# Kernel tuning notes

Hardware: AMD Instinct MI355X
Metric: run time of the kernel (lower is better)

## Reference

```python
import jax, jax.numpy as jnp
import numpy as np

NUM_BITS = 16           # continuousVarEncodingNumBits
THRESH = 4.0            # segmentActivationThreshold
K_SYN = 32              # numberOfSynapsesPerSegment
B, F, H, C = 512, 128, 8192, 10
E = F * NUM_BITS        # encodedFeatureSize = 2048


def _make_weight(key, n, p):
    # Dense int8-style weights: ~K_SYN random +/-1 synapses per neuron, rest 0.
    k1, k2 = jax.random.split(key)
    signs = jnp.where(jax.random.bernoulli(k1, 0.5, (n, p)), 1.0, -1.0)
    mask = jax.random.bernoulli(k2, K_SYN / p, (n, p))
    return (signs * mask).astype(jnp.float32)


def setup_inputs() -> dict:
    key = jax.random.key(0)
    ks = jax.random.split(key, 6)
    x = jax.random.uniform(ks[0], (B, F), dtype=jnp.float32)
    W0 = _make_weight(ks[1], H, E)   # layer 0: hidden x encoded
    W1 = _make_weight(ks[2], H, H)
    W2 = _make_weight(ks[3], H, H)
    # output connection matrix (numberOfHiddenLayers, hidden, classes); float variant
    outConn = jax.random.uniform(ks[4], (3, H, C), dtype=jnp.float32)
    return {"trainOrTest": 0, "x": x, "W0": W0, "W1": W1, "W2": W2, "outConn": outConn}


def reference(trainOrTest, x, W0, W1, W2, outConn):
    # thermometer bit-encoding of continuous vars: bit j on if x*NUM_BITS > j
    levels = jnp.arange(NUM_BITS, dtype=x.dtype)
    bits = jnp.where(x[:, :, None] * NUM_BITS > levels, 1.0, 0.0)  # (B, F, NUM_BITS)
    act = bits.reshape(x.shape[0], -1).astype(jnp.float32)          # (B, E)

    outAct = jnp.zeros((x.shape[0], outConn.shape[-1]), dtype=jnp.float32)
    for i, W in enumerate((W0, W1, W2)):
        z = act @ W.T                                   # segment sums (B, H)
        act = jnp.where(z >= THRESH, 1.0, 0.0)          # binary segment activation
        outAct = outAct + jnp.einsum('bh,hc->bc', act, outConn[i])
    preds = jnp.argmax(outAct, axis=-1)
    return preds, outAct
```

## Files before the change

kernel.cpp:

```cpp
#include <hip/hip_runtime.h>
#include <stdint.h>

#define BATCH   512
#define NFEAT   128
#define ESIZE   2048
#define HSIZE   8192
#define NCLS    10
#define THRESH_I 4
#define CAP     128
#define ROWB    64


__global__ __launch_bounds__(256) void encode_kernel(
    const float* __restrict__ x,
    uint8_t* __restrict__ aT0, uint8_t* __restrict__ aT1,
    uint8_t* __restrict__ aT2, uint8_t* __restrict__ aT3,
    int* __restrict__ counts,
    float* __restrict__ outAcc) {
  int t = blockIdx.x * 256 + threadIdx.x;
  if (t < BATCH * NCLS) outAcc[t] = 0.0f;
  else if (t < 5120 + 64)  aT0[(size_t)ESIZE * ROWB + (t - 5120)] = 0;
  else if (t < 5184 + 64)  aT1[(size_t)HSIZE * ROWB + (t - 5184)] = 0;
  else if (t < 5248 + 64)  aT2[(size_t)HSIZE * ROWB + (t - 5248)] = 0;
  else if (t < 5312 + 64)  aT3[(size_t)HSIZE * ROWB + (t - 5312)] = 0;
  counts[t] = 0;
  counts[t + 8192] = 0;
  counts[t + 16384] = 0;

  int wave = threadIdx.x >> 6;
  int lane = threadIdx.x & 63;
  int f = blockIdx.x * 4 + wave;
  if (f < NFEAT) {
    float u[8];
#pragma unroll
    for (int i = 0; i < 8; ++i)
      u[i] = x[(size_t)(lane + 64 * i) * NFEAT + f] * 16.0f;
#pragma unroll
    for (int j = 0; j < 16; ++j) {
      uint32_t byte = 0;
#pragma unroll
      for (int i = 0; i < 8; ++i)
        byte |= (u[i] > (float)j ? 1u : 0u) << i;
      aT0[(size_t)(f * 16 + j) * ROWB + lane] = (uint8_t)byte;
    }
  }
}

__global__ __launch_bounds__(256, 8) void convert_kernel(
    const float* __restrict__ W0, const float* __restrict__ W1,
    const float* __restrict__ W2,
    uint32_t* __restrict__ lists, int* __restrict__ counts) {
  int pair = (blockIdx.x * 256 + threadIdx.x) >> 6;
  int lane = threadIdx.x & 63;

  const float* W;
  int row, sloc, wid, P;
  if (pair < 16384) {
    W = W0; P = ESIZE;
    int s0 = pair * 2;
    row = s0 >> 2; sloc = s0 & 3; wid = row;
  } else if (pair < 16384 + 65536) {
    W = W1; P = HSIZE;
    int s0 = (pair - 16384) * 2;
    row = s0 >> 4; sloc = s0 & 15; wid = HSIZE + row;
  } else {
    W = W2; P = HSIZE;
    int s0 = (pair - 16384 - 65536) * 2;
    row = s0 >> 4; sloc = s0 & 15; wid = 2 * HSIZE + row;
  }

  const float4* w4 = (const float4*)(W + (size_t)row * P + (size_t)sloc * 512);
  float4 c0 = w4[lane];
  float4 c1 = w4[64 + lane];
  float4 c2 = w4[128 + lane];
  float4 c3 = w4[192 + lane];

  float v[16] = {c0.x, c0.y, c0.z, c0.w, c1.x, c1.y, c1.z, c1.w,
                 c2.x, c2.y, c2.z, c2.w, c3.x, c3.y, c3.z, c3.w};
  uint64_t m[16];
  int tt[16];
#pragma unroll
  for (int k = 0; k < 16; ++k) {
    m[k] = __ballot(v[k] != 0.0f);
    tt[k] = (int)__popcll(m[k]);
  }
  int total = 0;
#pragma unroll
  for (int k = 0; k < 16; ++k) total += tt[k];
  if (total == 0) return;

  int base = 0;
  if (lane == 0) base = atomicAdd(&counts[wid], total);
  base = __shfl(base, 0);

  uint64_t lmask = (lane == 0) ? 0ull : (~0ull >> (64 - lane));
  int ebase = sloc * 512;
  uint32_t* lp = lists + (size_t)wid * CAP;
  int off = base;
#pragma unroll
  for (int k = 0; k < 16; ++k) {
    if (v[k] != 0.0f) {
      int pos = off + (int)__popcll(m[k] & lmask);
      int e = ebase + (k >> 2) * 256 + (k & 3) + lane * 4;
      if (pos < CAP)
        lp[pos] = ((uint32_t)e << 1) | (v[k] < 0.0f ? 1u : 0u);
    }
    off += tt[k];
  }
}

__device__ __forceinline__ void proc_ent(uint32_t ent,
                                         const uint8_t* __restrict__ aIn,
                                         int lane, int* z) {
  uint32_t negm = (uint32_t)(-(int)(ent & 1u));
  uint32_t ee = ent >> 1;
  uint32_t byte = (uint32_t)aIn[(size_t)ee * ROWB + lane];
#pragma unroll
  for (int i = 0; i < 8; ++i) {
    uint32_t t = (byte >> i) & 1u;
    z[i] += (int)((t ^ negm) - negm);
  }
}

__device__ __forceinline__ void proc_comp_dense(float v, int ebase,
                                                const uint8_t* __restrict__ aIn,
                                                int lane, int* z) {
  uint64_t m = __ballot(v != 0.0f);
  if (m == 0ull) return;
  uint64_t pm = __ballot(v > 0.0f);
  do {
    uint32_t src = (uint32_t)__builtin_ctzll(m);
    m &= m - 1;
    int e = ebase + 4 * (int)src;
    uint32_t negm = ((pm >> src) & 1ull) ? 0u : 0xFFFFFFFFu;
    uint32_t byte = (uint32_t)aIn[(size_t)e * ROWB + lane];
#pragma unroll
    for (int i = 0; i < 8; ++i) {
      uint32_t t = (byte >> i) & 1u;
      z[i] += (int)((t ^ negm) - negm);
    }
  } while (m);
}

template <int P>
__global__ __launch_bounds__(512, 4) void layer_kernel(
    const uint32_t* __restrict__ lists, const int* __restrict__ counts,
    const float* __restrict__ W,
    const uint8_t* __restrict__ aIn, uint8_t* __restrict__ aOut) {
  int wave = threadIdx.x >> 6;
  int lane = threadIdx.x & 63;
  int hbase = blockIdx.x * 16 + wave * 2;
  const uint32_t SENT = (uint32_t)(P << 1);

  for (int r = 0; r < 2; ++r) {
    int h = hbase + r;
    int z[8];
#pragma unroll
    for (int i = 0; i < 8; ++i) z[i] = 0;

    int cnt = counts[h];
    if (cnt <= CAP) {
      const uint32_t* lp = lists + (size_t)h * CAP;
      int full = cnt & ~7;
      for (int i = 0; i < full; i += 8) {
        uint4 eA = *(const uint4*)(lp + i);
        uint4 eB = *(const uint4*)(lp + i + 4);
        proc_ent(eA.x, aIn, lane, z);
        proc_ent(eA.y, aIn, lane, z);
        proc_ent(eA.z, aIn, lane, z);
        proc_ent(eA.w, aIn, lane, z);
        proc_ent(eB.x, aIn, lane, z);
        proc_ent(eB.y, aIn, lane, z);
        proc_ent(eB.z, aIn, lane, z);
        proc_ent(eB.w, aIn, lane, z);
      }
      if (cnt & 7) {
        uint4 eA = *(const uint4*)(lp + full);
        uint4 eB = *(const uint4*)(lp + full + 4);
        uint32_t ee[8] = {eA.x, eA.y, eA.z, eA.w, eB.x, eB.y, eB.z, eB.w};
#pragma unroll
        for (int j = 0; j < 8; ++j)
          ee[j] = (full + j < cnt) ? ee[j] : SENT;
#pragma unroll
        for (int j = 0; j < 8; ++j) proc_ent(ee[j], aIn, lane, z);
      }
    } else {
      const float4* wrow = (const float4*)(W + (size_t)h * P) + lane;
      for (int it = 0; it < P / 256; ++it) {
        float4 wv = wrow[it * 64];
        int eb = it * 256;
        proc_comp_dense(wv.x, eb + 0, aIn, lane, z);
        proc_comp_dense(wv.y, eb + 1, aIn, lane, z);
        proc_comp_dense(wv.z, eb + 2, aIn, lane, z);
        proc_comp_dense(wv.w, eb + 3, aIn, lane, z);
      }
    }

    uint32_t ob = 0;
#pragma unroll
    for (int i = 0; i < 8; ++i)
      ob |= (z[i] >= THRESH_I ? 1u : 0u) << i;
    aOut[(size_t)h * ROWB + lane] = (uint8_t)ob;
  }
}

#define OCHUNK 128
__global__ __launch_bounds__(256, 4) void outacc_kernel(
    const float* __restrict__ outConn,
    const uint8_t* __restrict__ a1, const uint8_t* __restrict__ a2,
    const uint8_t* __restrict__ a3,
    float* __restrict__ outAcc) {
  __shared__ float shOC[OCHUNK][NCLS];
  __shared__ float shAcc[BATCH * NCLS];
  int tid = threadIdx.x;
  int gbase = blockIdx.x * OCHUNK;
  for (int idx = tid; idx < OCHUNK * NCLS; idx += 256)
    ((float*)shOC)[idx] = outConn[(size_t)gbase * NCLS + idx];
  for (int idx = tid; idx < BATCH * NCLS; idx += 256) shAcc[idx] = 0.0f;
  __syncthreads();

  int wave = tid >> 6;
  int lane = tid & 63;
  int layer = gbase >> 13;
  const uint8_t* aT = (layer == 0) ? a1 : (layer == 1) ? a2 : a3;
  int h0 = (gbase & (HSIZE - 1)) + wave * 32;

  float acc[8][NCLS];
#pragma unroll
  for (int i = 0; i < 8; ++i)
#pragma unroll
    for (int c = 0; c < NCLS; ++c) acc[i][c] = 0.0f;

  for (int r = 0; r < 32; ++r) {
    int row = h0 + r;
    uint32_t byte = (uint32_t)aT[(size_t)row * ROWB + lane];
    float bf[8];
#pragma unroll
    for (int i = 0; i < 8; ++i) bf[i] = (float)((byte >> i) & 1u);
    const float* oc = shOC[wave * 32 + r];
#pragma unroll
    for (int c = 0; c < NCLS; ++c) {
      float o = oc[c];
#pragma unroll
      for (int i = 0; i < 8; ++i) acc[i][c] += bf[i] * o;
    }
  }
#pragma unroll
  for (int i = 0; i < 8; ++i)
#pragma unroll
    for (int c = 0; c < NCLS; ++c)
      atomicAdd(&shAcc[(size_t)(lane + 64 * i) * NCLS + c], acc[i][c]);
  __syncthreads();
  for (int idx = tid; idx < BATCH * NCLS; idx += 256)
    atomicAdd(&outAcc[idx], shAcc[idx]);
}

__global__ __launch_bounds__(256) void final_kernel(
    const float* __restrict__ outAcc,
    int* __restrict__ preds,
    float* __restrict__ outF) {
  int b = blockIdx.x * 256 + threadIdx.x;
  if (b < BATCH) {
    float vals[NCLS];
#pragma unroll
    for (int c = 0; c < NCLS; ++c) vals[c] = outAcc[b * NCLS + c];
    float best = vals[0];
    int bi = 0;
#pragma unroll
    for (int c = 1; c < NCLS; ++c) {
      if (vals[c] > best) { best = vals[c]; bi = c; }
    }
    preds[b] = bi;
#pragma unroll
    for (int c = 0; c < NCLS; ++c) outF[b * NCLS + c] = vals[c];
  }
}

extern "C" void kernel_launch(void* const* d_in, const int* in_sizes, int n_in,
                              void* d_out, int out_size, void* d_ws, size_t ws_size,
                              hipStream_t stream) {
  const float* x       = (const float*)d_in[1];
  const float* W0      = (const float*)d_in[2];
  const float* W1      = (const float*)d_in[3];
  const float* W2      = (const float*)d_in[4];
  const float* outConn = (const float*)d_in[5];

  uint8_t* base = (uint8_t*)d_ws;
  uint8_t* aT0 = base;
  uint8_t* aT1 = base + 0x40000;
  uint8_t* aT2 = aT1 + 0x90000;
  uint8_t* aT3 = aT2 + 0x90000;
  uint32_t* lists = (uint32_t*)(aT3 + 0x90000);
  int* counts = (int*)((uint8_t*)lists +
                       ((size_t)3 * HSIZE * CAP + 64) * 4);
  float* outAcc = (float*)(counts + 3 * HSIZE);

  encode_kernel<<<32, 256, 0, stream>>>(x, aT0, aT1, aT2, aT3, counts, outAcc);
  convert_kernel<<<36864, 256, 0, stream>>>(W0, W1, W2, lists, counts);
  layer_kernel<ESIZE><<<512, 512, 0, stream>>>(
      lists, counts, W0, aT0, aT1);
  layer_kernel<HSIZE><<<512, 512, 0, stream>>>(
      lists + (size_t)HSIZE * CAP, counts + HSIZE, W1, aT1, aT2);
  layer_kernel<HSIZE><<<512, 512, 0, stream>>>(
      lists + (size_t)2 * HSIZE * CAP, counts + 2 * HSIZE, W2, aT2, aT3);
  outacc_kernel<<<192, 256, 0, stream>>>(outConn, aT1, aT2, aT3, outAcc);
  final_kernel<<<2, 256, 0, stream>>>(outAcc, (int*)d_out,
                                      (float*)d_out + BATCH);
}
```

Baseline: 651.4 us.

## Split weight conversion into bitmask scan and atomic-free compaction passes

Replaces the single convert kernel, which ballots each weight and does an atomicAdd per wave, with two passes. The first streams the dense float weights and packs each value into a 2-bit nonzero/sign mask. The second compacts each neuron's masks into its synapse list using a wave prefix scan, with no atomics. This removes atomic contention and the per-element ballots from the bandwidth-bound pass over the weights. It adds an extra mask buffer round-trip, one more launch, and serial ctz loops in the compaction.

After: 675.5 us. +3.7%, slower.

```diff
diff --git a/kernel.cpp b/kernel.cpp
--- a/kernel.cpp
+++ b/kernel.cpp
@@ -15,7 +15,6 @@
     const float* __restrict__ x,
     uint8_t* __restrict__ aT0, uint8_t* __restrict__ aT1,
     uint8_t* __restrict__ aT2, uint8_t* __restrict__ aT3,
-    int* __restrict__ counts,
     float* __restrict__ outAcc) {
   int t = blockIdx.x * 256 + threadIdx.x;
   if (t < BATCH * NCLS) outAcc[t] = 0.0f;
@@ -23,9 +22,6 @@
   else if (t < 5184 + 64)  aT1[(size_t)HSIZE * ROWB + (t - 5184)] = 0;
   else if (t < 5248 + 64)  aT2[(size_t)HSIZE * ROWB + (t - 5248)] = 0;
   else if (t < 5312 + 64)  aT3[(size_t)HSIZE * ROWB + (t - 5312)] = 0;
-  counts[t] = 0;
-  counts[t + 8192] = 0;
-  counts[t + 16384] = 0;
 
   int wave = threadIdx.x >> 6;
   int lane = threadIdx.x & 63;
@@ -46,67 +42,78 @@
   }
 }
 
-__global__ __launch_bounds__(256, 8) void convert_kernel(
+__global__ __launch_bounds__(256, 8) void scan_kernel(
     const float* __restrict__ W0, const float* __restrict__ W1,
-    const float* __restrict__ W2,
+    const float* __restrict__ W2, uint32_t* __restrict__ masks) {
+  int unit = (blockIdx.x * 256 + threadIdx.x) >> 6;
+  int lane = threadIdx.x & 63;
+  int s0 = unit * 2;
+  const float* W;
+  size_t off;
+  if (s0 < 16384)      { W = W0; off = (size_t)s0 * 1024; }
+  else if (s0 < 81920) { W = W1; off = (size_t)(s0 - 16384) * 1024; }
+  else                 { W = W2; off = (size_t)(s0 - 81920) * 1024; }
+  const float4* w4 = (const float4*)(W + off);
+
+  float4 c[8];
+#pragma unroll
+  for (int q = 0; q < 8; ++q) c[q] = w4[q * 64 + lane];
+
+  uint32_t out0 = 0, out1 = 0;
+#pragma unroll
+  for (int q = 0; q < 8; ++q) {
+    float v[4] = {c[q].x, c[q].y, c[q].z, c[q].w};
+    uint32_t w = 0;
+#pragma unroll
+    for (int k = 0; k < 4; ++k) {
+      uint32_t nz = (v[k] != 0.0f) ? 1u : 0u;
+      uint32_t sg = (v[k] < 0.0f) ? 1u : 0u;
+      w |= (nz | (sg << 1)) << (2 * ((q & 3) * 4 + k));
+    }
+    if (q < 4) out0 |= w; else out1 |= w;
+  }
+  masks[(size_t)s0 * 64 + lane] = out0;
+  masks[(size_t)(s0 + 1) * 64 + lane] = out1;
+}
+
+template <int S>
+__global__ __launch_bounds__(256, 8) void compact_kernel(
+    const uint32_t* __restrict__ masks, int stripeBase, int widBase,
     uint32_t* __restrict__ lists, int* __restrict__ counts) {
-  int pair = (blockIdx.x * 256 + threadIdx.x) >> 6;
+  int wrow = (blockIdx.x * 256 + threadIdx.x) >> 6;
   int lane = threadIdx.x & 63;
-
-  const float* W;
-  int row, sloc, wid, P;
-  if (pair < 16384) {
-    W = W0; P = ESIZE;
-    int s0 = pair * 2;
-    row = s0 >> 2; sloc = s0 & 3; wid = row;
-  } else if (pair < 16384 + 65536) {
-    W = W1; P = HSIZE;
-    int s0 = (pair - 16384) * 2;
-    row = s0 >> 4; sloc = s0 & 15; wid = HSIZE + row;
-  } else {
-    W = W2; P = HSIZE;
-    int s0 = (pair - 16384 - 65536) * 2;
-    row = s0 >> 4; sloc = s0 & 15; wid = 2 * HSIZE + row;
-  }
-
-  const float4* w4 = (const float4*)(W + (size_t)row * P + (size_t)sloc * 512);
-  float4 c0 = w4[lane];
-  float4 c1 = w4[64 + lane];
-  float4 c2 = w4[128 + lane];
-  float4 c3 = w4[192 + lane];
-
-  float v[16] = {c0.x, c0.y, c0.z, c0.w, c1.x, c1.y, c1.z, c1.w,
-                 c2.x, c2.y, c2.z, c2.w, c3.x, c3.y, c3.z, c3.w};
-  uint64_t m[16];
-  int tt[16];
-#pragma unroll
-  for (int k = 0; k < 16; ++k) {
-    m[k] = __ballot(v[k] != 0.0f);
-    tt[k] = (int)__popcll(m[k]);
-  }
-  int total = 0;
-#pragma unroll
-  for (int k = 0; k < 16; ++k) total += tt[k];
-  if (total == 0) return;
-
-  int base = 0;
-  if (lane == 0) base = atomicAdd(&counts[wid], total);
-  base = __shfl(base, 0);
-
-  uint64_t lmask = (lane == 0) ? 0ull : (~0ull >> (64 - lane));
-  int ebase = sloc * 512;
+  int wid = widBase + wrow;
+  int sbase = stripeBase + wrow * S;
+
+  uint32_t m[S];
+  int cnt = 0;
+#pragma unroll
+  for (int j = 0; j < S; ++j) {
+    m[j] = masks[(size_t)(sbase + j) * 64 + lane];
+    cnt += (int)__popc(m[j] & 0x55555555u);
+  }
+  int pre = cnt;
+#pragma unroll
+  for (int d = 1; d < 64; d <<= 1) {
+    int t = __shfl_up(pre, d);
+    if (lane >= d) pre += t;
+  }
+  int pos = pre - cnt;
   uint32_t* lp = lists + (size_t)wid * CAP;
-  int off = base;
-#pragma unroll
-  for (int k = 0; k < 16; ++k) {
-    if (v[k] != 0.0f) {
-      int pos = off + (int)__popcll(m[k] & lmask);
-      int e = ebase + (k >> 2) * 256 + (k & 3) + lane * 4;
-      if (pos < CAP)
-        lp[pos] = ((uint32_t)e << 1) | (v[k] < 0.0f ? 1u : 0u);
-    }
-    off += tt[k];
-  }
+#pragma unroll
+  for (int j = 0; j < S; ++j) {
+    uint32_t nzm = m[j] & 0x55555555u;
+    while (nzm) {
+      int b = __builtin_ctz(nzm);
+      nzm &= nzm - 1;
+      int i = b >> 1;
+      int e = j * 1024 + ((i >> 2) << 8) + lane * 4 + (i & 3);
+      uint32_t sign = (m[j] >> (b + 1)) & 1u;
+      if (pos < CAP) lp[pos] = ((uint32_t)e << 1) | sign;
+      ++pos;
+    }
+  }
+  if (lane == 63) counts[wid] = pre;
 }
 
 __device__ __forceinline__ void proc_ent(uint32_t ent,
@@ -294,9 +301,13 @@
   int* counts = (int*)((uint8_t*)lists +
                        ((size_t)3 * HSIZE * CAP + 64) * 4);
   float* outAcc = (float*)(counts + 3 * HSIZE);
-
-  encode_kernel<<<32, 256, 0, stream>>>(x, aT0, aT1, aT2, aT3, counts, outAcc);
-  convert_kernel<<<36864, 256, 0, stream>>>(W0, W1, W2, lists, counts);
+  uint32_t* masks = (uint32_t*)((uint8_t*)outAcc + BATCH * NCLS * 4 + 256);
+
+  encode_kernel<<<32, 256, 0, stream>>>(x, aT0, aT1, aT2, aT3, outAcc);
+  scan_kernel<<<18432, 256, 0, stream>>>(W0, W1, W2, masks);
+  compact_kernel<2><<<2048, 256, 0, stream>>>(masks, 0, 0, lists, counts);
+  compact_kernel<8><<<4096, 256, 0, stream>>>(masks, 16384, HSIZE, lists,
+                                              counts);
   layer_kernel<ESIZE><<<512, 512, 0, stream>>>(
       lists, counts, W0, aT0, aT1);
   layer_kernel<HSIZE><<<512, 512, 0, stream>>>(
```
